# Optimization experiments

Hardware: AMD Instinct MI355X
Metric: run time of the kernel (lower is better)

Reference implementation:

```python
import jax, jax.numpy as jnp
import numpy as np

B, S, E, H = 4, 2048, 1024, 16
D = E // H


def setup_inputs() -> dict:
    key = jax.random.key(0)
    ks = jax.random.split(key, 6)
    scale = 1.0 / np.sqrt(E).astype(np.float32)
    return {
        "x": jax.random.normal(ks[0], (B, S, E), jnp.float32),
        # positive entries -> cumsum normalizer is well conditioned
        "weight": jax.random.uniform(ks[1], (H, S), jnp.float32, 0.05, 1.0),
        "bias": jax.random.normal(ks[2], (H, S), jnp.float32) * 0.02,
        "inp_w": jax.random.normal(ks[3], (E, E), jnp.float32) * scale,
        "inp_b": jax.random.normal(ks[4], (E,), jnp.float32) * 0.02,
        "out_w": jax.random.normal(ks[5], (E, E), jnp.float32) * scale,
    }


def reference(x, weight, bias, inp_w, inp_b, out_w):
    Bx, Sx, Ex = x.shape
    Hx = weight.shape[0]
    Dx = Ex // Hx
    # input projection (torch Linear: x @ W.T + b)
    x = x @ inp_w.T + inp_b
    # (B,S,E) -> (B,E,S) -> (B,H,D,S)
    xh = x.transpose(0, 2, 1).reshape(Bx, Hx, Dx, Sx)
    # Toeplitz causal matrix per head: M[h,i,j] = weight[h, j-i] if j>=i else 0
    idx = jnp.arange(Sx)
    off = idx[None, :] - idx[:, None]  # (S,S)
    M = jnp.where(off >= 0, weight[:, off], jnp.zeros((), x.dtype))  # (H,S,S)
    # batched matmul over the sequence axis: y[b,h,d,t] = sum_s x[b,h,d,s] M[h,s,t]
    y = jnp.einsum('bhds,hst->bhdt', xh, M)
    # cumulative-sum normalization (do_toep_mean=True)
    norm = jnp.cumsum(weight, axis=-1)  # (H,S)
    y = y / norm[None, :, None, :]
    # per-head, per-position bias
    y = y + bias[None, :, None, :]
    # (B,H,D,S) -> (B,E,S) -> (B,S,E)
    y = y.reshape(Bx, Ex, Sx).transpose(0, 2, 1)
    # output projection (no bias)
    return y @ out_w.T
```

## Files before the change

kernel.cpp:

```cpp
#include <hip/hip_runtime.h>

typedef unsigned short u16;
typedef __attribute__((ext_vector_type(4))) float f32x4;
typedef __attribute__((ext_vector_type(8))) short short8;
typedef __attribute__((ext_vector_type(8))) __bf16 bf16x8;

__device__ __forceinline__ u16 f2bf(float f) {
  unsigned u = __builtin_bit_cast(unsigned, f);
  u = u + 0x7fffu + ((u >> 16) & 1u);
  return (u16)(u >> 16);
}

__device__ __forceinline__ void load_lds16(const void* g, void* l) {
  __builtin_amdgcn_global_load_lds((__attribute__((address_space(1))) void*)g,
                                   (__attribute__((address_space(3))) void*)l,
                                   16, 0, 0);
}

__global__ __launch_bounds__(256) void cast_f32_bf16(const float* __restrict__ in,
                                                     u16* __restrict__ out, int n4) {
  int i = blockIdx.x * 256 + threadIdx.x;
  if (i >= n4) return;
  const float4 v = ((const float4*)in)[i];
  ushort4 o;
  o.x = f2bf(v.x); o.y = f2bf(v.y); o.z = f2bf(v.z); o.w = f2bf(v.w);
  ((ushort4*)out)[i] = o;
}

__global__ __launch_bounds__(256) void prep_small(const float* __restrict__ inp_w,
                                                  const float* __restrict__ out_w,
                                                  const float* __restrict__ weight,
                                                  u16* __restrict__ Wb,
                                                  u16* __restrict__ OWb,
                                                  float* __restrict__ normB) {
  const int bx = blockIdx.x, tid = threadIdx.x;
  if (bx < 2048) {
    const float* src = (bx < 1024) ? inp_w : out_w;
    u16* dst = (bx < 1024) ? Wb : OWb;
    const int i = (bx & 1023) * 256 + tid;
    const float4 v = ((const float4*)src)[i];
    ushort4 o;
    o.x = f2bf(v.x); o.y = f2bf(v.y); o.z = f2bf(v.z); o.w = f2bf(v.w);
    ((ushort4*)dst)[i] = o;
    return;
  }
  const int h = bx - 2048;
  __shared__ float ts[256];
  float v[8];
  const float* src = weight + h * 2048 + tid * 8;
  float s = 0.f;
#pragma unroll
  for (int j = 0; j < 8; ++j) v[j] = src[j];
#pragma unroll
  for (int j = 0; j < 8; ++j) { s += v[j]; v[j] = s; }
  ts[tid] = s;
  __syncthreads();
  float x = s;
#pragma unroll
  for (int d = 1; d < 256; d <<= 1) {
    float y = (tid >= d) ? ts[tid - d] : 0.f;
    __syncthreads();
    x += y;
    ts[tid] = x;
    __syncthreads();
  }
  const float excl = x - s;
  float* dst = normB + h * 2048 + tid * 8;
#pragma unroll
  for (int j = 0; j < 8; ++j) dst[j] = excl + v[j];
}

__global__ __launch_bounds__(256) void build_V(const float* __restrict__ weight,
                                               u16* __restrict__ V) {
  const int h = blockIdx.x & 15, tb = blockIdx.x >> 4;
  __shared__ u16 wl[2048];
  const int tid = threadIdx.x;
#pragma unroll
  for (int j = 0; j < 8; ++j) wl[tid * 8 + j] = f2bf(weight[h * 2048 + tid * 8 + j]);
  __syncthreads();
#pragma unroll
  for (int i = 0; i < 8; ++i) {
    const int cid = i * 256 + tid;
    const int row = cid >> 4, c = cid & 15;
    const int t = tb * 128 + row;
    const int j0 = c * 8;
    unsigned v[8];
#pragma unroll
    for (int jj = 0; jj < 8; ++jj) {
      const int j = j0 + jj;
      v[jj] = (t >= j) ? (unsigned)wl[t - j] : 0u;
    }
    uint4 o;
    o.x = v[0] | (v[1] << 16); o.y = v[2] | (v[3] << 16);
    o.z = v[4] | (v[5] << 16); o.w = v[6] | (v[7] << 16);
    *(uint4*)(V + ((size_t)(h * 2048 + t)) * 128 + j0) = o;
  }
}

template <bool BIAS, bool F32OUT, int GX>
__global__ __launch_bounds__(256) void gemm_nt4(const u16* __restrict__ A,
                                                const u16* __restrict__ B,
                                                void* __restrict__ C,
                                                const float* __restrict__ bias,
                                                int K, int lda, int ldb, int ldc) {
  __shared__ __align__(16) u16 As[2][128 * 64];
  __shared__ __align__(16) u16 Bs[2][128 * 64];
  const int tid = threadIdx.x;
  const int lane = tid & 63, wv = tid >> 6;
  const int wm = wv >> 1, wn = wv & 1;
  const int l15 = lane & 15, g = lane >> 4;

  const int flat = (int)blockIdx.x;
  const int sw = (flat & 7) * 64 + (flat >> 3);
  const int m0 = (sw / GX) * 128, n0 = (sw % GX) * 128;

  const int NT = K >> 6;

  auto stage = [&](int t, int bi) {
    const int kt = t << 6;
#pragma unroll
    for (int i = 0; i < 4; ++i) {
      const int c = i * 256 + tid;
      const int row = c >> 3, cc = c & 7;
      load_lds16(A + (size_t)(m0 + row) * lda + kt + ((cc ^ (row & 7)) << 3),
                 &As[bi][i * 2048 + wv * 512]);
    }
#pragma unroll
    for (int i = 0; i < 4; ++i) {
      const int c = i * 256 + tid;
      const int row = c >> 3, cc = c & 7;
      load_lds16(B + (size_t)(n0 + row) * ldb + kt + ((cc ^ (row & 7)) << 3),
                 &Bs[bi][i * 2048 + wv * 512]);
    }
  };

  f32x4 acc[4][4] = {};
  stage(0, 0);
  __syncthreads();
  int cur = 0;
  for (int t = 0; t < NT; ++t) {
    if (t + 1 < NT) stage(t + 1, cur ^ 1);
#pragma unroll
    for (int kh = 0; kh < 2; ++kh) {
      bf16x8 af[4], bf[4];
#pragma unroll
      for (int mf = 0; mf < 4; ++mf) {
        const int row = wm * 64 + mf * 16 + l15;
        af[mf] = *(const bf16x8*)(&As[cur][row * 64 + ((((kh << 2) + g) ^ (row & 7)) << 3)]);
      }
#pragma unroll
      for (int nf = 0; nf < 4; ++nf) {
        const int row = wn * 64 + nf * 16 + l15;
        bf[nf] = *(const bf16x8*)(&Bs[cur][row * 64 + ((((kh << 2) + g) ^ (row & 7)) << 3)]);
      }
      __builtin_amdgcn_s_setprio(1);
#pragma unroll
      for (int mf = 0; mf < 4; ++mf)
#pragma unroll
        for (int nf = 0; nf < 4; ++nf)
          acc[mf][nf] = __builtin_amdgcn_mfma_f32_16x16x32_bf16(af[mf], bf[nf],
                                                                acc[mf][nf], 0, 0, 0);
      __builtin_amdgcn_s_setprio(0);
    }
    __syncthreads();
    cur ^= 1;
  }

#pragma unroll
  for (int mf = 0; mf < 4; ++mf) {
#pragma unroll
    for (int r = 0; r < 4; ++r) {
      const int row = m0 + wm * 64 + mf * 16 + g * 4 + r;
      const float bb = BIAS ? bias[row] : 0.f;
#pragma unroll
      for (int nf = 0; nf < 4; ++nf) {
        const int col = n0 + wn * 64 + nf * 16 + l15;
        const float v = acc[mf][nf][r] + bb;
        if (F32OUT)
          ((float*)C)[(size_t)row * ldc + col] = v;
        else
          ((u16*)C)[(size_t)row * ldc + col] = f2bf(v);
      }
    }
  }
}

__global__ __launch_bounds__(256) void toep_conv(const u16* __restrict__ X1t,
                                                 const u16* __restrict__ V,
                                                 const float* __restrict__ normB,
                                                 const float* __restrict__ biasB,
                                                 u16* __restrict__ Y2b) {
  __shared__ __align__(16) u16 As[3][128 * 64];
  __shared__ __align__(16) u16 Xs[3][64 * 64];
  const int tid = threadIdx.x;
  const int lane = tid & 63, wv = tid >> 6;
  const int l15 = lane & 15, g = lane >> 4;

  const int x = (int)blockIdx.x;
  const int h = (x & 7) + 8 * ((x >> 3) & 1);
  const int pb = x >> 4;
  const int pair = pb & 7, b = pb >> 3;

  const u16* Vh = V + (size_t)h * 2048 * 128;
  const u16* Xrow = X1t + (size_t)h * 64 * 8192 + b * 2048;

#pragma unroll 1
  for (int ti = 0; ti < 2; ++ti) {
    const int tt = ti ? pair : 15 - pair;
    const int t0 = tt * 128;
    const int Q = (tt + 1) * 2;
    f32x4 acc[2][4] = {};

    auto stage = [&](int q, int bufi) {
      const int st = q >> 1, k = q & 1;
      const u16* Ab = Vh + (size_t)(tt - st) * 128 * 128 + k * 64;
#pragma unroll
      for (int i = 0; i < 4; ++i) {
        const int c = i * 256 + tid;
        const int row = c >> 3, cc = c & 7;
        load_lds16(Ab + row * 128 + ((cc ^ (row & 7)) * 8),
                   &As[bufi][i * 2048 + wv * 512]);
      }
      const int s0 = st * 128 + k * 64;
#pragma unroll
      for (int i = 0; i < 2; ++i) {
        const int c = i * 256 + tid;
        const int row = c >> 3, cc = c & 7;
        load_lds16(Xrow + (size_t)row * 8192 + s0 + ((cc ^ (row & 7)) * 8),
                   &Xs[bufi][i * 2048 + wv * 512]);
      }
    };

    stage(0, 0);
    if (Q > 1) stage(1, 1);
    asm volatile("s_waitcnt vmcnt(6)" ::: "memory");
    __builtin_amdgcn_sched_barrier(0);
    __builtin_amdgcn_s_barrier();
    asm volatile("" ::: "memory");

    int cur = 0;
    for (int q = 0; q < Q; ++q) {
      if (q + 2 < Q) stage(q + 2, (q + 2) % 3);
#pragma unroll
      for (int ks = 0; ks < 2; ++ks) {
        bf16x8 af[2];
#pragma unroll
        for (int tf = 0; tf < 2; ++tf) {
          const int row = wv * 32 + tf * 16 + l15;
          af[tf] = *(const bf16x8*)(&As[cur][row * 64 + (((ks * 4 + g) ^ (row & 7)) * 8)]);
        }
#pragma unroll
        for (int nf = 0; nf < 4; ++nf) {
          const int row = nf * 16 + l15;
          const bf16x8 bv = *(const bf16x8*)(&Xs[cur][row * 64 + (((ks * 4 + g) ^ (row & 7)) * 8)]);
#pragma unroll
          for (int tf = 0; tf < 2; ++tf)
            acc[tf][nf] = __builtin_amdgcn_mfma_f32_16x16x32_bf16(af[tf], bv,
                                                                  acc[tf][nf], 0, 0, 0);
        }
      }
      if (q + 2 < Q)      asm volatile("s_waitcnt vmcnt(6)" ::: "memory");
      else if (q + 1 < Q) asm volatile("s_waitcnt vmcnt(0)" ::: "memory");
      __builtin_amdgcn_sched_barrier(0);
      __builtin_amdgcn_s_barrier();
      asm volatile("" ::: "memory");
      cur = (cur == 2) ? 0 : cur + 1;
    }

#pragma unroll
    for (int tf = 0; tf < 2; ++tf) {
#pragma unroll
      for (int r = 0; r < 4; ++r) {
        const int t = t0 + wv * 32 + tf * 16 + g * 4 + r;
        const float inv = 1.0f / normB[h * 2048 + t];
        const float bb = biasB[h * 2048 + t];
#pragma unroll
        for (int nf = 0; nf < 4; ++nf) {
          const int d = nf * 16 + l15;
          Y2b[(size_t)(b * 2048 + t) * 1024 + h * 64 + d] = f2bf(acc[tf][nf][r] * inv + bb);
        }
      }
    }
  }
}

extern "C" void kernel_launch(void* const* d_in, const int* in_sizes, int n_in,
                              void* d_out, int out_size, void* d_ws, size_t ws_size,
                              hipStream_t stream) {
  (void)in_sizes; (void)n_in; (void)out_size; (void)ws_size;
  const float* x      = (const float*)d_in[0];
  const float* weight = (const float*)d_in[1];
  const float* biasB  = (const float*)d_in[2];
  const float* inp_w  = (const float*)d_in[3];
  const float* inp_b  = (const float*)d_in[4];
  const float* out_w  = (const float*)d_in[5];

  char* ws = (char*)d_ws;
  u16* Xb    = (u16*)(ws + 0);
  u16* X1t   = (u16*)(ws + (size_t)(16u << 20));
  u16* Y2b   = (u16*)(ws + (size_t)(32u << 20));
  u16* Wb    = (u16*)(ws + (size_t)(48u << 20));
  u16* OWb   = (u16*)(ws + (size_t)(50u << 20));
  float* normB = (float*)(ws + (size_t)(53u << 20));
  u16* Vt    = (u16*)(ws + (size_t)(56u << 20));

  cast_f32_bf16<<<8192, 256, 0, stream>>>(x, Xb, 2097152);
  prep_small<<<2064, 256, 0, stream>>>(inp_w, out_w, weight, Wb, OWb, normB);
  build_V<<<256, 256, 0, stream>>>(weight, Vt);

  gemm_nt4<true, false, 64><<<512, 256, 0, stream>>>(
      Wb, Xb, (void*)X1t, inp_b, 1024, 1024, 1024, 8192);

  toep_conv<<<512, 256, 0, stream>>>(X1t, Vt, normB, biasB, Y2b);

  gemm_nt4<false, true, 8><<<512, 256, 0, stream>>>(
      Y2b, OWb, d_out, nullptr, 1024, 1024, 1024, 1024);
}
```

Measured before the change: 102.2 us.

## Rewrite projection GEMMs as 128x256 tiles with triple-buffered ping-pong pipeline

Replaces the 128x128 double-buffered GEMM with a 512-thread, 128x256-tile kernel that keeps three LDS stages and prefetches two tiles ahead. Global-to-LDS loads are interleaved with MFMA phases using explicit barriers, waitcnt, and priority hints. Block-to-tile mapping also changes, with an M-fast order for the input projection. This aims to hide memory latency and raise MFMA utilisation, at the cost of 144 KB of LDS per block, fewer blocks per CU, and fragile hand-tuned synchronisation.

```diff
diff --git a/kernel.cpp b/kernel.cpp
--- a/kernel.cpp
+++ b/kernel.cpp
@@ -15,6 +15,10 @@
   __builtin_amdgcn_global_load_lds((__attribute__((address_space(1))) void*)g,
                                    (__attribute__((address_space(3))) void*)l,
                                    16, 0, 0);
+}
+
+__device__ __forceinline__ f32x4 MF(bf16x8 a, bf16x8 b, f32x4 c) {
+  return __builtin_amdgcn_mfma_f32_16x16x32_bf16(a, b, c, 0, 0, 0);
 }
 
 __global__ __launch_bounds__(256) void cast_f32_bf16(const float* __restrict__ in,
@@ -97,73 +101,134 @@
   }
 }
 
-template <bool BIAS, bool F32OUT, int GX>
-__global__ __launch_bounds__(256) void gemm_nt4(const u16* __restrict__ A,
-                                                const u16* __restrict__ B,
-                                                void* __restrict__ C,
-                                                const float* __restrict__ bias,
-                                                int K, int lda, int ldb, int ldc) {
-  __shared__ __align__(16) u16 As[2][128 * 64];
-  __shared__ __align__(16) u16 Bs[2][128 * 64];
+template <bool BIAS, bool F32OUT, bool MFAST, int D>
+__global__ __launch_bounds__(512) void gemm_p4(const u16* __restrict__ A,
+                                               const u16* __restrict__ B,
+                                               void* __restrict__ C,
+                                               const float* __restrict__ bias,
+                                               int K, int lda, int ldb, int ldc) {
+  __shared__ __align__(16) u16 As[3][128 * 64];
+  __shared__ __align__(16) u16 Bs[3][256 * 64];
   const int tid = threadIdx.x;
   const int lane = tid & 63, wv = tid >> 6;
-  const int wm = wv >> 1, wn = wv & 1;
+  const int wm = wv >> 2, wn = wv & 3;
   const int l15 = lane & 15, g = lane >> 4;
+  const int r7 = l15 & 7;
 
   const int flat = (int)blockIdx.x;
-  const int sw = (flat & 7) * 64 + (flat >> 3);
-  const int m0 = (sw / GX) * 128, n0 = (sw % GX) * 128;
+  const int sw = (flat & 7) * 32 + (flat >> 3);
+  const int m0 = (MFAST ? (sw % D) : (sw / D)) * 128;
+  const int n0 = (MFAST ? (sw / D) : (sw % D)) * 256;
 
   const int NT = K >> 6;
 
-  auto stage = [&](int t, int bi) {
-    const int kt = t << 6;
-#pragma unroll
-    for (int i = 0; i < 4; ++i) {
-      const int c = i * 256 + tid;
-      const int row = c >> 3, cc = c & 7;
-      load_lds16(A + (size_t)(m0 + row) * lda + kt + ((cc ^ (row & 7)) << 3),
-                 &As[bi][i * 2048 + wv * 512]);
-    }
-#pragma unroll
-    for (int i = 0; i < 4; ++i) {
-      const int c = i * 256 + tid;
-      const int row = c >> 3, cc = c & 7;
-      load_lds16(B + (size_t)(n0 + row) * ldb + kt + ((cc ^ (row & 7)) << 3),
-                 &Bs[bi][i * 2048 + wv * 512]);
-    }
+  auto stA = [&](int t, int bi, int i) {
+    const int c = i * 512 + tid, row = c >> 3, cc = c & 7;
+    load_lds16(A + (size_t)(m0 + row) * lda + (t << 6) + ((cc ^ (row & 7)) << 3),
+               &As[bi][i * 4096 + wv * 512]);
   };
+  auto stB = [&](int t, int bi, int i) {
+    const int c = i * 512 + tid, row = c >> 3, cc = c & 7;
+    load_lds16(B + (size_t)(n0 + row) * ldb + (t << 6) + ((cc ^ (row & 7)) << 3),
+               &Bs[bi][i * 4096 + wv * 512]);
+  };
+
+  int aRow[4], bRow[4];
+#pragma unroll
+  for (int i = 0; i < 4; ++i) {
+    aRow[i] = (wm * 64 + i * 16 + l15) * 64;
+    bRow[i] = (wn * 64 + i * 16 + l15) * 64;
+  }
+  const int sl0 = (g ^ r7) << 3;
+  const int sl1 = ((4 + g) ^ r7) << 3;
 
   f32x4 acc[4][4] = {};
-  stage(0, 0);
-  __syncthreads();
+
+  stA(0, 0, 0); stA(0, 0, 1);
+  stB(0, 0, 0); stB(0, 0, 1); stB(0, 0, 2); stB(0, 0, 3);
+  stA(1, 1, 0); stA(1, 1, 1);
+  stB(1, 1, 0); stB(1, 1, 1); stB(1, 1, 2); stB(1, 1, 3);
+  asm volatile("s_waitcnt vmcnt(6)" ::: "memory");
+  __builtin_amdgcn_sched_barrier(0);
+  __builtin_amdgcn_s_barrier();
+  __builtin_amdgcn_sched_barrier(0);
+
   int cur = 0;
+#pragma unroll 1
   for (int t = 0; t < NT; ++t) {
-    if (t + 1 < NT) stage(t + 1, cur ^ 1);
-#pragma unroll
-    for (int kh = 0; kh < 2; ++kh) {
-      bf16x8 af[4], bf[4];
-#pragma unroll
-      for (int mf = 0; mf < 4; ++mf) {
-        const int row = wm * 64 + mf * 16 + l15;
-        af[mf] = *(const bf16x8*)(&As[cur][row * 64 + ((((kh << 2) + g) ^ (row & 7)) << 3)]);
-      }
-#pragma unroll
-      for (int nf = 0; nf < 4; ++nf) {
-        const int row = wn * 64 + nf * 16 + l15;
-        bf[nf] = *(const bf16x8*)(&Bs[cur][row * 64 + ((((kh << 2) + g) ^ (row & 7)) << 3)]);
-      }
-      __builtin_amdgcn_s_setprio(1);
-#pragma unroll
-      for (int mf = 0; mf < 4; ++mf)
-#pragma unroll
-        for (int nf = 0; nf < 4; ++nf)
-          acc[mf][nf] = __builtin_amdgcn_mfma_f32_16x16x32_bf16(af[mf], bf[nf],
-                                                                acc[mf][nf], 0, 0, 0);
-      __builtin_amdgcn_s_setprio(0);
-    }
-    __syncthreads();
-    cur ^= 1;
+    const u16* Ac = &As[cur][0];
+    const u16* Bc = &Bs[cur][0];
+    const int nb = (cur == 0) ? 2 : cur - 1;
+    const bool pf = (t + 2 < NT);
+    bf16x8 af0, af1, af2, af3, b0, b1;
+
+    af0 = *(const bf16x8*)(Ac + aRow[0] + sl0);
+    af1 = *(const bf16x8*)(Ac + aRow[1] + sl0);
+    af2 = *(const bf16x8*)(Ac + aRow[2] + sl0);
+    af3 = *(const bf16x8*)(Ac + aRow[3] + sl0);
+    b0  = *(const bf16x8*)(Bc + bRow[0] + sl0);
+    b1  = *(const bf16x8*)(Bc + bRow[1] + sl0);
+    if (pf) { stB(t + 2, nb, 0); stB(t + 2, nb, 1); }
+    __builtin_amdgcn_s_barrier();
+    asm volatile("s_waitcnt lgkmcnt(0)" ::: "memory");
+    __builtin_amdgcn_sched_barrier(0);
+    __builtin_amdgcn_s_setprio(1);
+    acc[0][0] = MF(af0, b0, acc[0][0]); acc[1][0] = MF(af1, b0, acc[1][0]);
+    acc[2][0] = MF(af2, b0, acc[2][0]); acc[3][0] = MF(af3, b0, acc[3][0]);
+    acc[0][1] = MF(af0, b1, acc[0][1]); acc[1][1] = MF(af1, b1, acc[1][1]);
+    acc[2][1] = MF(af2, b1, acc[2][1]); acc[3][1] = MF(af3, b1, acc[3][1]);
+    __builtin_amdgcn_s_setprio(0);
+    __builtin_amdgcn_s_barrier();
+
+    b0 = *(const bf16x8*)(Bc + bRow[2] + sl0);
+    b1 = *(const bf16x8*)(Bc + bRow[3] + sl0);
+    if (pf) { stB(t + 2, nb, 2); stB(t + 2, nb, 3); }
+    __builtin_amdgcn_s_barrier();
+    asm volatile("s_waitcnt lgkmcnt(0)" ::: "memory");
+    __builtin_amdgcn_sched_barrier(0);
+    __builtin_amdgcn_s_setprio(1);
+    acc[0][2] = MF(af0, b0, acc[0][2]); acc[1][2] = MF(af1, b0, acc[1][2]);
+    acc[2][2] = MF(af2, b0, acc[2][2]); acc[3][2] = MF(af3, b0, acc[3][2]);
+    acc[0][3] = MF(af0, b1, acc[0][3]); acc[1][3] = MF(af1, b1, acc[1][3]);
+    acc[2][3] = MF(af2, b1, acc[2][3]); acc[3][3] = MF(af3, b1, acc[3][3]);
+    __builtin_amdgcn_s_setprio(0);
+    __builtin_amdgcn_s_barrier();
+
+    af0 = *(const bf16x8*)(Ac + aRow[0] + sl1);
+    af1 = *(const bf16x8*)(Ac + aRow[1] + sl1);
+    af2 = *(const bf16x8*)(Ac + aRow[2] + sl1);
+    af3 = *(const bf16x8*)(Ac + aRow[3] + sl1);
+    b0  = *(const bf16x8*)(Bc + bRow[0] + sl1);
+    b1  = *(const bf16x8*)(Bc + bRow[1] + sl1);
+    if (pf) { stA(t + 2, nb, 0); stA(t + 2, nb, 1); }
+    __builtin_amdgcn_s_barrier();
+    asm volatile("s_waitcnt lgkmcnt(0)" ::: "memory");
+    __builtin_amdgcn_sched_barrier(0);
+    __builtin_amdgcn_s_setprio(1);
+    acc[0][0] = MF(af0, b0, acc[0][0]); acc[1][0] = MF(af1, b0, acc[1][0]);
+    acc[2][0] = MF(af2, b0, acc[2][0]); acc[3][0] = MF(af3, b0, acc[3][0]);
+    acc[0][1] = MF(af0, b1, acc[0][1]); acc[1][1] = MF(af1, b1, acc[1][1]);
+    acc[2][1] = MF(af2, b1, acc[2][1]); acc[3][1] = MF(af3, b1, acc[3][1]);
+    __builtin_amdgcn_s_setprio(0);
+    __builtin_amdgcn_s_barrier();
+
+    b0 = *(const bf16x8*)(Bc + bRow[2] + sl1);
+    b1 = *(const bf16x8*)(Bc + bRow[3] + sl1);
+    __builtin_amdgcn_s_barrier();
+    asm volatile("s_waitcnt lgkmcnt(0)" ::: "memory");
+    __builtin_amdgcn_sched_barrier(0);
+    __builtin_amdgcn_s_setprio(1);
+    acc[0][2] = MF(af0, b0, acc[0][2]); acc[1][2] = MF(af1, b0, acc[1][2]);
+    acc[2][2] = MF(af2, b0, acc[2][2]); acc[3][2] = MF(af3, b0, acc[3][2]);
+    acc[0][3] = MF(af0, b1, acc[0][3]); acc[1][3] = MF(af1, b1, acc[1][3]);
+    acc[2][3] = MF(af2, b1, acc[2][3]); acc[3][3] = MF(af3, b1, acc[3][3]);
+    __builtin_amdgcn_s_setprio(0);
+    if (pf)                { asm volatile("s_waitcnt vmcnt(6)" ::: "memory"); }
+    else if (t + 1 < NT)   { asm volatile("s_waitcnt vmcnt(0)" ::: "memory"); }
+    __builtin_amdgcn_sched_barrier(0);
+    __builtin_amdgcn_s_barrier();
+    __builtin_amdgcn_sched_barrier(0);
+    cur = (cur == 2) ? 0 : cur + 1;
   }
 
 #pragma unroll
@@ -308,11 +373,11 @@
   prep_small<<<2064, 256, 0, stream>>>(inp_w, out_w, weight, Wb, OWb, normB);
   build_V<<<256, 256, 0, stream>>>(weight, Vt);
 
-  gemm_nt4<true, false, 64><<<512, 256, 0, stream>>>(
+  gemm_p4<true, false, true, 8><<<256, 512, 0, stream>>>(
       Wb, Xb, (void*)X1t, inp_b, 1024, 1024, 1024, 8192);
 
   toep_conv<<<512, 256, 0, stream>>>(X1t, Vt, normB, biasB, Y2b);
 
-  gemm_nt4<false, true, 8><<<512, 256, 0, stream>>>(
+  gemm_p4<false, true, false, 4><<<256, 512, 0, stream>>>(
       Y2b, OWb, d_out, nullptr, 1024, 1024, 1024, 1024);
 }
```

New measurement: 108.0 us. 1.06x slower.
